# Performance work log

Measured on AMD Instinct MI355X. Metric: run time of the kernel, lower is better.

## Reference

```python
import jax, jax.numpy as jnp
import numpy as np

NEG_SLOPE = 0.01  # torch F.leaky_relu default


def setup_inputs() -> dict:
    key = jax.random.key(0)
    k1, k2, k3, k4, k5 = jax.random.split(key, 5)
    N, E, IN_DIM, OUT_DIM = 100000, 1600000, 128, 64
    h = jax.random.normal(k1, (N, IN_DIM), dtype=jnp.float32)
    src = jax.random.randint(k2, (E,), 0, N, dtype=jnp.int64)
    dst = jax.random.randint(k3, (E,), 0, N, dtype=jnp.int64)
    # xavier_normal-ish scaled params
    W1 = jax.random.normal(k4, (OUT_DIM, IN_DIM), dtype=jnp.float32) * (2.0 / (IN_DIM + OUT_DIM)) ** 0.5
    Wa = jax.random.normal(k5, (1, 2 * OUT_DIM), dtype=jnp.float32) * (2.0 / (2 * OUT_DIM + 1)) ** 0.5
    return {"h": h, "src": src, "dst": dst, "W1": W1, "Wa": Wa}


def reference(h, src, dst, W1, Wa):
    N = h.shape[0]
    D = W1.shape[0]
    z = h @ W1.T  # [N, D]
    z_src = z[src]  # [E, D] gather
    z_dst = z[dst]  # [E, D] gather
    a_src, a_dst = Wa[0, :D], Wa[0, D:]
    # attn_fc(concat(z_src, z_dst)) == z_src@a_src + z_dst@a_dst
    e = z_src @ a_src + z_dst @ a_dst  # [E]
    e = jnp.where(e >= 0, e, NEG_SLOPE * e)  # leaky_relu
    # segment softmax over incoming edges of each dst node
    e_max = jax.ops.segment_max(e, dst, num_segments=N)
    e_max = jnp.where(jnp.isfinite(e_max), e_max, 0.0)  # empty segments
    e_exp = jnp.exp(e - e_max[dst])
    denom = jax.ops.segment_sum(e_exp, dst, num_segments=N)
    alpha = e_exp / jnp.maximum(denom, 1e-16)[dst]  # [E]
    # weighted scatter-sum of source messages
    h_out = jax.ops.segment_sum(alpha[:, None] * z_src, dst, num_segments=N)  # [N, D]
    return h_out
```

## Files before the change

kernel.cpp:

```cpp
#include <hip/hip_runtime.h>
#include <hip/hip_bf16.h>

#define NEG_SLOPE 0.01f
#define NPB 512
#define CHUNK 4096

typedef __attribute__((ext_vector_type(8))) short short8;
typedef __attribute__((ext_vector_type(4))) float f32x4;

__device__ __forceinline__ unsigned short f2bf_rne(float f) {
    unsigned u = __float_as_uint(f);
    u += 0x7FFFu + ((u >> 16) & 1u);
    return (unsigned short)(u >> 16);
}

__global__ __launch_bounds__(256) void k_gemm(
    const float* __restrict__ h, const float* __restrict__ W1,
    const float* __restrict__ Wa, unsigned short* __restrict__ zb,
    float* __restrict__ s, float* __restrict__ t, int N)
{
    __shared__ __align__(16) short hsb[64 * 128];
    __shared__ __align__(16) short wsb[64 * 128];
    const int tid = threadIdx.x;
    const int nb = blockIdx.x * 64;

    const float4* __restrict__ h4 = (const float4*)h;
    const float4* __restrict__ W14 = (const float4*)W1;
#pragma unroll
    for (int it = 0; it < 4; ++it) {
        const int q = tid + it * 256;
        const int r = q >> 4, cb = q & 15;
        const int sidx = r * 128 + ((cb * 8) ^ ((r & 7) << 3));
        {
            const int n = nb + r;
            float4 v0 = make_float4(0.f,0.f,0.f,0.f), v1 = v0;
            if (n < N) { v0 = h4[(size_t)n * 32 + cb * 2]; v1 = h4[(size_t)n * 32 + cb * 2 + 1]; }
            short8 o;
            o[0]=f2bf_rne(v0.x); o[1]=f2bf_rne(v0.y); o[2]=f2bf_rne(v0.z); o[3]=f2bf_rne(v0.w);
            o[4]=f2bf_rne(v1.x); o[5]=f2bf_rne(v1.y); o[6]=f2bf_rne(v1.z); o[7]=f2bf_rne(v1.w);
            *(short8*)&hsb[sidx] = o;
        }
        {
            float4 v0 = W14[(size_t)r * 32 + cb * 2];
            float4 v1 = W14[(size_t)r * 32 + cb * 2 + 1];
            short8 o;
            o[0]=f2bf_rne(v0.x); o[1]=f2bf_rne(v0.y); o[2]=f2bf_rne(v0.z); o[3]=f2bf_rne(v0.w);
            o[4]=f2bf_rne(v1.x); o[5]=f2bf_rne(v1.y); o[6]=f2bf_rne(v1.z); o[7]=f2bf_rne(v1.w);
            *(short8*)&wsb[sidx] = o;
        }
    }
    __syncthreads();

    const int w  = tid >> 6;
    const int l  = tid & 63;
    const int lr = l & 15;
    const int lc = l >> 4;
    f32x4 acc[4];
#pragma unroll
    for (int ni = 0; ni < 4; ++ni) acc[ni] = (f32x4){0.f, 0.f, 0.f, 0.f};

#pragma unroll
    for (int ks = 0; ks < 4; ++ks) {
        const int kcb = ks * 4 + lc;
        const short8 af = *(const short8*)&hsb[(w * 16 + lr) * 128 + ((kcb * 8) ^ ((lr & 7) << 3))];
#pragma unroll
        for (int ni = 0; ni < 4; ++ni) {
            const int wr = ni * 16 + lr;
            const short8 bf = *(const short8*)&wsb[wr * 128 + ((kcb * 8) ^ ((wr & 7) << 3))];
            acc[ni] = __builtin_amdgcn_mfma_f32_16x16x32_bf16(af, bf, acc[ni], 0, 0, 0);
        }
    }

    float asrc[4], adst[4];
#pragma unroll
    for (int ni = 0; ni < 4; ++ni) {
        asrc[ni] = Wa[ni * 16 + lr];
        adst[ni] = Wa[64 + ni * 16 + lr];
    }
#pragma unroll
    for (int r = 0; r < 4; ++r) {
        float ps = 0.f, pt = 0.f;
#pragma unroll
        for (int ni = 0; ni < 4; ++ni) {
            ps = fmaf(acc[ni][r], asrc[ni], ps);
            pt = fmaf(acc[ni][r], adst[ni], pt);
        }
#pragma unroll
        for (int m = 1; m < 16; m <<= 1) {
            ps += __shfl_xor(ps, m);
            pt += __shfl_xor(pt, m);
        }
        const int node = nb + w * 16 + lc * 4 + r;
        if (lr == 0 && node < N) { s[node] = ps; t[node] = pt; }
    }
#pragma unroll
    for (int ni = 0; ni < 4; ++ni)
#pragma unroll
        for (int r = 0; r < 4; ++r) {
            const int node = nb + w * 16 + lc * 4 + r;
            if (node < N) zb[(size_t)node * 64 + ni * 16 + lr] = f2bf_rne(acc[ni][r]);
        }
}

__global__ __launch_bounds__(256) void k_part2(
    const int* __restrict__ src, const int* __restrict__ dst,
    unsigned* __restrict__ gcur, unsigned* __restrict__ table,
    int E, int NBKT, int BCAP)
{
    __shared__ unsigned cnt[256];
    __shared__ unsigned exc[256];
    __shared__ unsigned sbuf[256];
    __shared__ unsigned gbaseb[256];
    __shared__ unsigned stage[CHUNK];
    __shared__ unsigned short bkt[CHUNK];

    const int t = threadIdx.x;
    const int e0 = blockIdx.x * CHUNK;
    const int nE = min(CHUNK, E - e0);

    cnt[t] = 0u;
    __syncthreads();
    for (int i = t; i < nE; i += 256)
        atomicAdd(&cnt[(unsigned)dst[e0 + i] >> 9], 1u);
    __syncthreads();

    const unsigned myc = cnt[t];
    if (t < NBKT && myc > 0u) gbaseb[t] = atomicAdd(&gcur[t], myc);

    sbuf[t] = myc;
    __syncthreads();
    for (int off = 1; off < 256; off <<= 1) {
        unsigned x = (t >= off) ? sbuf[t - off] : 0u;
        __syncthreads();
        sbuf[t] += x;
        __syncthreads();
    }
    exc[t] = sbuf[t] - myc;
    __syncthreads();
    cnt[t] = 0u;
    __syncthreads();

    for (int i = t; i < nE; i += 256) {
        const unsigned d = (unsigned)dst[e0 + i];
        const unsigned b = d >> 9;
        const unsigned pos = exc[b] + atomicAdd(&cnt[b], 1u);
        stage[pos] = ((unsigned)src[e0 + i] << 9) | (d & 511u);
        bkt[pos] = (unsigned short)b;
    }
    __syncthreads();

    for (int i = t; i < nE; i += 256) {
        const unsigned b = bkt[i];
        const unsigned off = gbaseb[b] + ((unsigned)i - exc[b]);
        if (off < (unsigned)BCAP)
            table[(size_t)b * BCAP + off] = stage[i];
    }
}

__global__ __launch_bounds__(256) void k_scanb(
    const unsigned* __restrict__ gcur, unsigned* __restrict__ gbase,
    int NBKT, int BCAP)
{
    __shared__ unsigned sbuf[256];
    const int t = threadIdx.x;
    unsigned c = (t < NBKT) ? min(gcur[t], (unsigned)BCAP) : 0u;
    sbuf[t] = c;
    __syncthreads();
    for (int off = 1; off < 256; off <<= 1) {
        unsigned x = (t >= off) ? sbuf[t - off] : 0u;
        __syncthreads();
        sbuf[t] += x;
        __syncthreads();
    }
    if (t < NBKT) gbase[t] = sbuf[t] - c;
}

__global__ __launch_bounds__(256) void k_sortb2(
    const unsigned* __restrict__ table, const unsigned* __restrict__ gcur,
    const unsigned* __restrict__ gbase, unsigned* __restrict__ edge_src,
    unsigned* __restrict__ offsets, unsigned* __restrict__ counts,
    int N, int BCAP)
{
    __shared__ unsigned ncnt[NPB];
    __shared__ unsigned nexc[NPB];
    __shared__ unsigned sbuf[NPB];
    const int b = blockIdx.x;
    const int t = threadIdx.x;
    const int bc = min((int)gcur[b], BCAP);
    const unsigned base = gbase[b];
    const size_t tb = (size_t)b * BCAP;

    ncnt[t] = 0u; ncnt[t + 256] = 0u;
    __syncthreads();
    for (int i = t; i < bc; i += 256)
        atomicAdd(&ncnt[table[tb + i] & 511u], 1u);
    __syncthreads();

    const unsigned c0 = ncnt[t], c1 = ncnt[t + 256];
    sbuf[t] = c0; sbuf[t + 256] = c1;
    __syncthreads();
    for (int off = 1; off < NPB; off <<= 1) {
        unsigned x0 = (t >= off) ? sbuf[t - off] : 0u;
        unsigned x1 = (t + 256 >= off) ? sbuf[t + 256 - off] : 0u;
        __syncthreads();
        sbuf[t] += x0; sbuf[t + 256] += x1;
        __syncthreads();
    }
    nexc[t] = sbuf[t] - c0; nexc[t + 256] = sbuf[t + 256] - c1;
    __syncthreads();

    {
        const int n0 = b * NPB + t, n1 = n0 + 256;
        if (n0 < N) { offsets[n0] = base + nexc[t];        counts[n0] = c0; }
        if (n1 < N) { offsets[n1] = base + nexc[t + 256];  counts[n1] = c1; }
    }
    ncnt[t] = 0u; ncnt[t + 256] = 0u;
    __syncthreads();

    for (int i = t; i < bc; i += 256) {
        const unsigned v = table[tb + i];
        const unsigned l = v & 511u;
        const unsigned pos = nexc[l] + atomicAdd(&ncnt[l], 1u);
        edge_src[base + pos] = v >> 9;
    }
}

__global__ __launch_bounds__(256) void k_node(
    const unsigned* __restrict__ offsets, const unsigned* __restrict__ counts,
    const unsigned* __restrict__ edge_src,
    const float* __restrict__ s, const float* __restrict__ t,
    const unsigned short* __restrict__ zb, float* __restrict__ out, int N)
{
    const int tid = threadIdx.x;
    const int node = blockIdx.x * 16 + (tid >> 4);
    if (node >= N) return;
    const int wl    = tid & 63;
    const int gbase = wl & ~15;
    const int sub   = wl & 15;
    const int g2    = sub >> 3;
    const int l8    = sub & 7;

    const unsigned beg = offsets[node];
    const int cnt = (int)counts[node];
    if (cnt == 0) {
        if (sub < 8) {
            const float4 zz = make_float4(0.f, 0.f, 0.f, 0.f);
            *(float4*)&out[(size_t)node * 64 + sub * 8]     = zz;
            *(float4*)&out[(size_t)node * 64 + sub * 8 + 4] = zz;
        }
        return;
    }

    const float tn = t[node];
    float dl = 0.f;
    float acc[8] = {0.f, 0.f, 0.f, 0.f, 0.f, 0.f, 0.f, 0.f};

    for (int base = 0; base < cnt; base += 16) {
        const int rem = min(16, cnt - base);
        int sj = 0;
        float p = 0.f;
        if (sub < rem) {
            sj = (int)edge_src[beg + base + sub];
            float e = s[sj] + tn;
            e = (e >= 0.f) ? e : NEG_SLOPE * e;
            p = __expf(e);
            dl += p;
        }
        int jc = rem - g2 * 8;
        if (jc > 8) jc = 8;
        for (int k = 0; k < jc; ++k) {
            const int j = g2 * 8 + k;
            const float pj  = __shfl(p, gbase + j);
            const int   sjj = __shfl(sj, gbase + j);
            const uint4 v = *(const uint4*)&zb[(size_t)sjj * 64 + l8 * 8];
#define UNPK(u, d0) \
            acc[d0]     = fmaf(pj, __uint_as_float((u) << 16),          acc[d0]); \
            acc[d0 + 1] = fmaf(pj, __uint_as_float((u) & 0xFFFF0000u), acc[d0 + 1]);
            UNPK(v.x, 0) UNPK(v.y, 2) UNPK(v.z, 4) UNPK(v.w, 6)
#undef UNPK
        }
    }

#pragma unroll
    for (int c = 0; c < 8; ++c)
        acc[c] += __shfl_xor(acc[c], 8);
    float den = dl;
#pragma unroll
    for (int m = 1; m < 16; m <<= 1) den += __shfl_xor(den, m);

    if (sub < 8) {
        const float inv = 1.f / fmaxf(den, 1e-16f);
        float4 o0 = make_float4(acc[0] * inv, acc[1] * inv, acc[2] * inv, acc[3] * inv);
        float4 o1 = make_float4(acc[4] * inv, acc[5] * inv, acc[6] * inv, acc[7] * inv);
        *(float4*)&out[(size_t)node * 64 + sub * 8]     = o0;
        *(float4*)&out[(size_t)node * 64 + sub * 8 + 4] = o1;
    }
}

extern "C" void kernel_launch(void* const* d_in, const int* in_sizes, int n_in,
                              void* d_out, int out_size, void* d_ws, size_t ws_size,
                              hipStream_t stream) {
    const float* h   = (const float*)d_in[0];
    const int*   src = (const int*)d_in[1];
    const int*   dst = (const int*)d_in[2];
    const float* W1  = (const float*)d_in[3];
    const float* Wa  = (const float*)d_in[4];
    float* out = (float*)d_out;

    const int N = in_sizes[0] / 128;
    const int E = in_sizes[1];
    const int NBKT = (N + NPB - 1) / NPB;
    const int meanb = (E + NBKT - 1) / NBKT;
    int slack = 24 * (int)sqrtf((float)meanb) + 64;
    const int BCAP = meanb + slack;

    unsigned short* zb = (unsigned short*)d_ws;
    float*    s        = (float*)(zb + (size_t)N * 64);
    float*    t        = s + N;
    unsigned* gcur     = (unsigned*)(t + N);
    unsigned* gbase    = gcur + NBKT;
    unsigned* offsets  = gbase + NBKT;
    unsigned* counts   = offsets + N;
    unsigned* edge_src = counts + N;
    unsigned* table    = edge_src + E;

    hipMemsetAsync(gcur, 0, (size_t)NBKT * sizeof(unsigned), stream);

    k_gemm<<<(N + 63) / 64, 256, 0, stream>>>(h, W1, Wa, zb, s, t, N);
    k_part2<<<(E + CHUNK - 1) / CHUNK, 256, 0, stream>>>(src, dst, gcur, table, E, NBKT, BCAP);
    k_scanb<<<1, 256, 0, stream>>>(gcur, gbase, NBKT, BCAP);
    k_sortb2<<<NBKT, 256, 0, stream>>>(table, gcur, gbase, edge_src, offsets, counts, N, BCAP);
    k_node<<<(N + 15) / 16, 256, 0, stream>>>(offsets, counts, edge_src, s, t, zb, out, N);
}
```

Baseline: 114.0 us.

## Merge GEMM and edge partition into one launch; fully unroll node gather loop

The projection GEMM and the edge bucket-partition kernels are independent, so they are combined into a single launch. Blocks below G1 do the GEMM and the rest do partitioning, with their shared memory overlaid in a union. This removes one launch boundary and lets the memory-bound partition run alongside the GEMM. In the node aggregation kernel the per-group gather loop is fully unrolled to 8 iterations and the row offset is hoisted. Out-of-range slots read row 0 with zero weight, which adds redundant loads for partial groups.

Measured after the change: 105.3 us. 1.08x faster.

```diff
diff --git a/kernel.cpp b/kernel.cpp
--- a/kernel.cpp
+++ b/kernel.cpp
@@ -14,146 +14,143 @@
     return (unsigned short)(u >> 16);
 }
 
-__global__ __launch_bounds__(256) void k_gemm(
+__global__ __launch_bounds__(256) void k_gp(
     const float* __restrict__ h, const float* __restrict__ W1,
     const float* __restrict__ Wa, unsigned short* __restrict__ zb,
-    float* __restrict__ s, float* __restrict__ t, int N)
-{
-    __shared__ __align__(16) short hsb[64 * 128];
-    __shared__ __align__(16) short wsb[64 * 128];
-    const int tid = threadIdx.x;
-    const int nb = blockIdx.x * 64;
-
-    const float4* __restrict__ h4 = (const float4*)h;
-    const float4* __restrict__ W14 = (const float4*)W1;
-#pragma unroll
-    for (int it = 0; it < 4; ++it) {
-        const int q = tid + it * 256;
-        const int r = q >> 4, cb = q & 15;
-        const int sidx = r * 128 + ((cb * 8) ^ ((r & 7) << 3));
-        {
-            const int n = nb + r;
-            float4 v0 = make_float4(0.f,0.f,0.f,0.f), v1 = v0;
-            if (n < N) { v0 = h4[(size_t)n * 32 + cb * 2]; v1 = h4[(size_t)n * 32 + cb * 2 + 1]; }
-            short8 o;
-            o[0]=f2bf_rne(v0.x); o[1]=f2bf_rne(v0.y); o[2]=f2bf_rne(v0.z); o[3]=f2bf_rne(v0.w);
-            o[4]=f2bf_rne(v1.x); o[5]=f2bf_rne(v1.y); o[6]=f2bf_rne(v1.z); o[7]=f2bf_rne(v1.w);
-            *(short8*)&hsb[sidx] = o;
-        }
-        {
-            float4 v0 = W14[(size_t)r * 32 + cb * 2];
-            float4 v1 = W14[(size_t)r * 32 + cb * 2 + 1];
-            short8 o;
-            o[0]=f2bf_rne(v0.x); o[1]=f2bf_rne(v0.y); o[2]=f2bf_rne(v0.z); o[3]=f2bf_rne(v0.w);
-            o[4]=f2bf_rne(v1.x); o[5]=f2bf_rne(v1.y); o[6]=f2bf_rne(v1.z); o[7]=f2bf_rne(v1.w);
-            *(short8*)&wsb[sidx] = o;
-        }
-    }
-    __syncthreads();
-
-    const int w  = tid >> 6;
-    const int l  = tid & 63;
-    const int lr = l & 15;
-    const int lc = l >> 4;
-    f32x4 acc[4];
-#pragma unroll
-    for (int ni = 0; ni < 4; ++ni) acc[ni] = (f32x4){0.f, 0.f, 0.f, 0.f};
-
-#pragma unroll
-    for (int ks = 0; ks < 4; ++ks) {
-        const int kcb = ks * 4 + lc;
-        const short8 af = *(const short8*)&hsb[(w * 16 + lr) * 128 + ((kcb * 8) ^ ((lr & 7) << 3))];
-#pragma unroll
-        for (int ni = 0; ni < 4; ++ni) {
-            const int wr = ni * 16 + lr;
-            const short8 bf = *(const short8*)&wsb[wr * 128 + ((kcb * 8) ^ ((wr & 7) << 3))];
-            acc[ni] = __builtin_amdgcn_mfma_f32_16x16x32_bf16(af, bf, acc[ni], 0, 0, 0);
-        }
-    }
-
-    float asrc[4], adst[4];
-#pragma unroll
-    for (int ni = 0; ni < 4; ++ni) {
-        asrc[ni] = Wa[ni * 16 + lr];
-        adst[ni] = Wa[64 + ni * 16 + lr];
-    }
-#pragma unroll
-    for (int r = 0; r < 4; ++r) {
-        float ps = 0.f, pt = 0.f;
-#pragma unroll
-        for (int ni = 0; ni < 4; ++ni) {
-            ps = fmaf(acc[ni][r], asrc[ni], ps);
-            pt = fmaf(acc[ni][r], adst[ni], pt);
-        }
-#pragma unroll
-        for (int m = 1; m < 16; m <<= 1) {
-            ps += __shfl_xor(ps, m);
-            pt += __shfl_xor(pt, m);
-        }
-        const int node = nb + w * 16 + lc * 4 + r;
-        if (lr == 0 && node < N) { s[node] = ps; t[node] = pt; }
-    }
-#pragma unroll
-    for (int ni = 0; ni < 4; ++ni)
-#pragma unroll
-        for (int r = 0; r < 4; ++r) {
-            const int node = nb + w * 16 + lc * 4 + r;
-            if (node < N) zb[(size_t)node * 64 + ni * 16 + lr] = f2bf_rne(acc[ni][r]);
-        }
-}
-
-__global__ __launch_bounds__(256) void k_part2(
+    float* __restrict__ s, float* __restrict__ t, int N, int G1,
     const int* __restrict__ src, const int* __restrict__ dst,
     unsigned* __restrict__ gcur, unsigned* __restrict__ table,
     int E, int NBKT, int BCAP)
 {
-    __shared__ unsigned cnt[256];
-    __shared__ unsigned exc[256];
-    __shared__ unsigned sbuf[256];
-    __shared__ unsigned gbaseb[256];
-    __shared__ unsigned stage[CHUNK];
-    __shared__ unsigned short bkt[CHUNK];
-
-    const int t = threadIdx.x;
-    const int e0 = blockIdx.x * CHUNK;
-    const int nE = min(CHUNK, E - e0);
-
-    cnt[t] = 0u;
-    __syncthreads();
-    for (int i = t; i < nE; i += 256)
-        atomicAdd(&cnt[(unsigned)dst[e0 + i] >> 9], 1u);
-    __syncthreads();
-
-    const unsigned myc = cnt[t];
-    if (t < NBKT && myc > 0u) gbaseb[t] = atomicAdd(&gcur[t], myc);
-
-    sbuf[t] = myc;
-    __syncthreads();
-    for (int off = 1; off < 256; off <<= 1) {
-        unsigned x = (t >= off) ? sbuf[t - off] : 0u;
-        __syncthreads();
-        sbuf[t] += x;
-        __syncthreads();
-    }
-    exc[t] = sbuf[t] - myc;
-    __syncthreads();
-    cnt[t] = 0u;
-    __syncthreads();
-
-    for (int i = t; i < nE; i += 256) {
-        const unsigned d = (unsigned)dst[e0 + i];
-        const unsigned b = d >> 9;
-        const unsigned pos = exc[b] + atomicAdd(&cnt[b], 1u);
-        stage[pos] = ((unsigned)src[e0 + i] << 9) | (d & 511u);
-        bkt[pos] = (unsigned short)b;
-    }
-    __syncthreads();
-
-    for (int i = t; i < nE; i += 256) {
-        const unsigned b = bkt[i];
-        const unsigned off = gbaseb[b] + ((unsigned)i - exc[b]);
-        if (off < (unsigned)BCAP)
-            table[(size_t)b * BCAP + off] = stage[i];
+    __shared__ __align__(16) union SM {
+        struct { short hsb[64 * 128]; short wsb[64 * 128]; } g;
+        struct {
+            unsigned cnt[256]; unsigned exc[256]; unsigned sbuf[256];
+            unsigned gbaseb[256]; unsigned stage[CHUNK];
+            unsigned short bkt[CHUNK];
+        } p;
+    } sm;
+    const int tid = threadIdx.x;
+
+    if (blockIdx.x < (unsigned)G1) {
+        const int nb = blockIdx.x * 64;
+        const float4* __restrict__ h4 = (const float4*)h;
+        const float4* __restrict__ W14 = (const float4*)W1;
+#pragma unroll
+        for (int it = 0; it < 4; ++it) {
+            const int q = tid + it * 256;
+            const int r = q >> 4, cb = q & 15;
+            const int sidx = r * 128 + ((cb * 8) ^ ((r & 7) << 3));
+            {
+                const int n = nb + r;
+                float4 v0 = make_float4(0.f,0.f,0.f,0.f), v1 = v0;
+                if (n < N) { v0 = h4[(size_t)n * 32 + cb * 2]; v1 = h4[(size_t)n * 32 + cb * 2 + 1]; }
+                short8 o;
+                o[0]=f2bf_rne(v0.x); o[1]=f2bf_rne(v0.y); o[2]=f2bf_rne(v0.z); o[3]=f2bf_rne(v0.w);
+                o[4]=f2bf_rne(v1.x); o[5]=f2bf_rne(v1.y); o[6]=f2bf_rne(v1.z); o[7]=f2bf_rne(v1.w);
+                *(short8*)&sm.g.hsb[sidx] = o;
+            }
+            {
+                float4 v0 = W14[(size_t)r * 32 + cb * 2];
+                float4 v1 = W14[(size_t)r * 32 + cb * 2 + 1];
+                short8 o;
+                o[0]=f2bf_rne(v0.x); o[1]=f2bf_rne(v0.y); o[2]=f2bf_rne(v0.z); o[3]=f2bf_rne(v0.w);
+                o[4]=f2bf_rne(v1.x); o[5]=f2bf_rne(v1.y); o[6]=f2bf_rne(v1.z); o[7]=f2bf_rne(v1.w);
+                *(short8*)&sm.g.wsb[sidx] = o;
+            }
+        }
+        __syncthreads();
+
+        const int w  = tid >> 6;
+        const int l  = tid & 63;
+        const int lr = l & 15;
+        const int lc = l >> 4;
+        f32x4 acc[4];
+#pragma unroll
+        for (int ni = 0; ni < 4; ++ni) acc[ni] = (f32x4){0.f, 0.f, 0.f, 0.f};
+
+#pragma unroll
+        for (int ks = 0; ks < 4; ++ks) {
+            const int kcb = ks * 4 + lc;
+            const short8 af = *(const short8*)&sm.g.hsb[(w * 16 + lr) * 128 + ((kcb * 8) ^ ((lr & 7) << 3))];
+#pragma unroll
+            for (int ni = 0; ni < 4; ++ni) {
+                const int wr = ni * 16 + lr;
+                const short8 bf = *(const short8*)&sm.g.wsb[wr * 128 + ((kcb * 8) ^ ((wr & 7) << 3))];
+                acc[ni] = __builtin_amdgcn_mfma_f32_16x16x32_bf16(af, bf, acc[ni], 0, 0, 0);
+            }
+        }
+
+        float asrc[4], adst[4];
+#pragma unroll
+        for (int ni = 0; ni < 4; ++ni) {
+            asrc[ni] = Wa[ni * 16 + lr];
+            adst[ni] = Wa[64 + ni * 16 + lr];
+        }
+#pragma unroll
+        for (int r = 0; r < 4; ++r) {
+            float ps = 0.f, pt = 0.f;
+#pragma unroll
+            for (int ni = 0; ni < 4; ++ni) {
+                ps = fmaf(acc[ni][r], asrc[ni], ps);
+                pt = fmaf(acc[ni][r], adst[ni], pt);
+            }
+#pragma unroll
+            for (int m = 1; m < 16; m <<= 1) {
+                ps += __shfl_xor(ps, m);
+                pt += __shfl_xor(pt, m);
+            }
+            const int node = nb + w * 16 + lc * 4 + r;
+            if (lr == 0 && node < N) { s[node] = ps; t[node] = pt; }
+        }
+#pragma unroll
+        for (int ni = 0; ni < 4; ++ni)
+#pragma unroll
+            for (int r = 0; r < 4; ++r) {
+                const int node = nb + w * 16 + lc * 4 + r;
+                if (node < N) zb[(size_t)node * 64 + ni * 16 + lr] = f2bf_rne(acc[ni][r]);
+            }
+    } else {
+        const int e0 = (blockIdx.x - G1) * CHUNK;
+        const int nE = min(CHUNK, E - e0);
+
+        sm.p.cnt[tid] = 0u;
+        __syncthreads();
+        for (int i = tid; i < nE; i += 256)
+            atomicAdd(&sm.p.cnt[(unsigned)dst[e0 + i] >> 9], 1u);
+        __syncthreads();
+
+        const unsigned myc = sm.p.cnt[tid];
+        if (tid < NBKT && myc > 0u) sm.p.gbaseb[tid] = atomicAdd(&gcur[tid], myc);
+
+        sm.p.sbuf[tid] = myc;
+        __syncthreads();
+        for (int off = 1; off < 256; off <<= 1) {
+            unsigned x = (tid >= off) ? sm.p.sbuf[tid - off] : 0u;
+            __syncthreads();
+            sm.p.sbuf[tid] += x;
+            __syncthreads();
+        }
+        sm.p.exc[tid] = sm.p.sbuf[tid] - myc;
+        __syncthreads();
+        sm.p.cnt[tid] = 0u;
+        __syncthreads();
+
+        for (int i = tid; i < nE; i += 256) {
+            const unsigned d = (unsigned)dst[e0 + i];
+            const unsigned b = d >> 9;
+            const unsigned pos = sm.p.exc[b] + atomicAdd(&sm.p.cnt[b], 1u);
+            sm.p.stage[pos] = ((unsigned)src[e0 + i] << 9) | (d & 511u);
+            sm.p.bkt[pos] = (unsigned short)b;
+        }
+        __syncthreads();
+
+        for (int i = tid; i < nE; i += 256) {
+            const unsigned b = sm.p.bkt[i];
+            const unsigned off = sm.p.gbaseb[b] + ((unsigned)i - sm.p.exc[b]);
+            if (off < (unsigned)BCAP)
+                table[(size_t)b * BCAP + off] = sm.p.stage[i];
+        }
     }
 }
 
@@ -252,6 +249,7 @@
     }
 
     const float tn = t[node];
+    const unsigned short* __restrict__ zrow = zb + l8 * 8;
     float dl = 0.f;
     float acc[8] = {0.f, 0.f, 0.f, 0.f, 0.f, 0.f, 0.f, 0.f};
 
@@ -266,13 +264,12 @@
             p = __expf(e);
             dl += p;
         }
-        int jc = rem - g2 * 8;
-        if (jc > 8) jc = 8;
-        for (int k = 0; k < jc; ++k) {
+#pragma unroll
+        for (int k = 0; k < 8; ++k) {
             const int j = g2 * 8 + k;
             const float pj  = __shfl(p, gbase + j);
             const int   sjj = __shfl(sj, gbase + j);
-            const uint4 v = *(const uint4*)&zb[(size_t)sjj * 64 + l8 * 8];
+            const uint4 v = *(const uint4*)&zrow[(size_t)sjj * 64];
 #define UNPK(u, d0) \
             acc[d0]     = fmaf(pj, __uint_as_float((u) << 16),          acc[d0]); \
             acc[d0 + 1] = fmaf(pj, __uint_as_float((u) & 0xFFFF0000u), acc[d0 + 1]);
@@ -314,6 +311,9 @@
     int slack = 24 * (int)sqrtf((float)meanb) + 64;
     const int BCAP = meanb + slack;
 
+    const int G1 = (N + 63) / 64;
+    const int G2 = (E + CHUNK - 1) / CHUNK;
+
     unsigned short* zb = (unsigned short*)d_ws;
     float*    s        = (float*)(zb + (size_t)N * 64);
     float*    t        = s + N;
@@ -326,8 +326,8 @@
 
     hipMemsetAsync(gcur, 0, (size_t)NBKT * sizeof(unsigned), stream);
 
-    k_gemm<<<(N + 63) / 64, 256, 0, stream>>>(h, W1, Wa, zb, s, t, N);
-    k_part2<<<(E + CHUNK - 1) / CHUNK, 256, 0, stream>>>(src, dst, gcur, table, E, NBKT, BCAP);
+    k_gp<<<G1 + G2, 256, 0, stream>>>(h, W1, Wa, zb, s, t, N, G1,
+                                      src, dst, gcur, table, E, NBKT, BCAP);
     k_scanb<<<1, 256, 0, stream>>>(gcur, gbase, NBKT, BCAP);
     k_sortb2<<<NBKT, 256, 0, stream>>>(table, gcur, gbase, edge_src, offsets, counts, N, BCAP);
     k_node<<<(N + 15) / 16, 256, 0, stream>>>(offsets, counts, edge_src, s, t, zb, out, N);
```
